# Kernel optimization log

Measured on AMD Instinct MI355X. Metric: run time of the kernel, lower is better.

## Reference

```python
import jax, jax.numpy as jnp
import numpy as np

D_STATE = 16
D_CONV = 4
TOKEN = 8
GROUPS = 4
EPS = 1e-5


def _gn(x, w, b):
    # GroupNorm(GROUPS) over [B,C,H,W]
    B, C, H, W = x.shape
    xr = x.reshape(B, GROUPS, C // GROUPS, H * W)
    mu = xr.mean((2, 3), keepdims=True)
    var = xr.var((2, 3), keepdims=True)
    xn = ((xr - mu) * jax.lax.rsqrt(var + EPS)).reshape(B, C, H, W)
    return xn * w[None, :, None, None] + b[None, :, None, None]


def _mamba(x, in_w, conv_w, conv_b, xp_w, dt_w, dt_b, A_log, Dp, out_w, dt_rank):
    # mamba_ssm Mamba forward: x [B, L, d_model]
    Bn, L, _ = x.shape
    d_inner = conv_w.shape[0]
    xz = jnp.einsum('bld,ed->ble', x, in_w)          # [B,L,2*d_inner]
    xc, z = jnp.split(xz, 2, axis=-1)
    # causal depthwise conv1d (pad left d_conv-1)
    xt = jnp.pad(jnp.transpose(xc, (0, 2, 1)), ((0, 0), (0, 0), (D_CONV - 1, 0)))
    xt = jax.lax.conv_general_dilated(xt, conv_w[:, None, :], (1,), 'VALID',
                                      dimension_numbers=('NCH', 'OIH', 'NCH'),
                                      feature_group_count=d_inner)
    xc = jax.nn.silu(jnp.transpose(xt, (0, 2, 1)) + conv_b)
    dbl = jnp.einsum('ble,fe->blf', xc, xp_w)        # [B,L,dt_rank+2*d_state]
    dt = dbl[..., :dt_rank]
    Bm = dbl[..., dt_rank:dt_rank + D_STATE]
    Cm = dbl[..., dt_rank + D_STATE:]
    delta = jax.nn.softplus(jnp.einsum('blr,er->ble', dt, dt_w) + dt_b)
    A = -jnp.exp(A_log)                              # [d_inner, d_state]

    def step(h, inp):
        u_t, d_t, b_t, c_t = inp                     # [B,d_inner],[B,d_inner],[B,d_state],[B,d_state]
        dA = jnp.exp(d_t[..., None] * A)
        h = h * dA + (d_t * u_t)[..., None] * b_t[:, None, :]
        return h, jnp.sum(h * c_t[:, None, :], axis=-1)

    xs = (jnp.transpose(xc, (1, 0, 2)), jnp.transpose(delta, (1, 0, 2)),
          jnp.transpose(Bm, (1, 0, 2)), jnp.transpose(Cm, (1, 0, 2)))
    h0 = jnp.zeros((Bn, d_inner, D_STATE), x.dtype)
    _, ys = jax.lax.scan(step, h0, xs)
    y = (jnp.transpose(ys, (1, 0, 2)) + xc * Dp) * jax.nn.silu(z)
    return jnp.einsum('ble,de->bld', y, out_w)


def _mamba_params(key, d_model, dt_rank):
    d_inner = 2 * d_model
    ks = jax.random.split(key, 5)
    p = {}
    p['in_w'] = jax.random.normal(ks[0], (2 * d_inner, d_model)) / np.sqrt(d_model).astype(np.float32)
    p['conv_w'] = jax.random.normal(ks[1], (d_inner, D_CONV)) * 0.3
    p['conv_b'] = jnp.zeros((d_inner,))
    p['xp_w'] = jax.random.normal(ks[2], (dt_rank + 2 * D_STATE, d_inner)) / np.sqrt(d_inner).astype(np.float32)
    p['dt_w'] = jax.random.normal(ks[3], (d_inner, dt_rank)) / np.sqrt(dt_rank).astype(np.float32)
    p['dt_b'] = jnp.full((d_inner,), float(np.log(np.expm1(0.01))))
    p['A_log'] = jnp.log(jnp.broadcast_to(jnp.arange(1, D_STATE + 1, dtype=jnp.float32), (d_inner, D_STATE)))
    p['D'] = jnp.ones((d_inner,))
    p['out_w'] = jax.random.normal(ks[4], (d_model, d_inner)) / np.sqrt(d_inner).astype(np.float32)
    return p


def setup_inputs() -> dict:
    key = jax.random.key(0)
    k1, k2, k3 = jax.random.split(key, 3)
    B, C, H, W = 2, 64, 128, 128
    inp = {'x': jax.random.normal(k1, (B, C, H, W), dtype=jnp.float32)}
    spa = _mamba_params(k2, C, 4)
    spe = _mamba_params(k3, C // TOKEN, 1)
    for n, p in (('spa', spa), ('spe', spe)):
        for k, v in p.items():
            inp[f'{n}_{k}'] = v
    inp['spa_gn_w'] = jnp.ones((C,)); inp['spa_gn_b'] = jnp.zeros((C,))
    inp['spe_gn_w'] = jnp.ones((C,)); inp['spe_gn_b'] = jnp.zeros((C,))
    inp['fuse_w'] = jnp.full((2,), 0.5)
    return inp


def reference(x, spa_in_w, spa_conv_w, spa_conv_b, spa_xp_w, spa_dt_w, spa_dt_b,
              spa_A_log, spa_D, spa_out_w, spe_in_w, spe_conv_w, spe_conv_b,
              spe_xp_w, spe_dt_w, spe_dt_b, spe_A_log, spe_D, spe_out_w,
              spa_gn_w, spa_gn_b, spe_gn_w, spe_gn_b, fuse_w):
    B, C, H, W = x.shape
    # SpaMamba: scan over flattened spatial sequence
    xs = jnp.transpose(x, (0, 2, 3, 1)).reshape(B, H * W, C)
    ys = _mamba(xs, spa_in_w, spa_conv_w, spa_conv_b, spa_xp_w, spa_dt_w, spa_dt_b,
                spa_A_log, spa_D, spa_out_w, 4)
    spa = jnp.transpose(ys.reshape(B, H, W, C), (0, 3, 1, 2))
    spa = jax.nn.silu(_gn(spa, spa_gn_w, spa_gn_b)) + x
    # SpeMamba: scan over channel tokens per pixel (C == TOKEN * gc, no padding)
    gc = C // TOKEN
    xe = jnp.transpose(x, (0, 2, 3, 1)).reshape(B * H * W, TOKEN, gc)
    ye = _mamba(xe, spe_in_w, spe_conv_w, spe_conv_b, spe_xp_w, spe_dt_w, spe_dt_b,
                spe_A_log, spe_D, spe_out_w, 1)
    spe = jnp.transpose(ye.reshape(B, H, W, C), (0, 3, 1, 2))
    spe = jax.nn.silu(_gn(spe, spe_gn_w, spe_gn_b)) + x
    w = jax.nn.softmax(fuse_w)
    return spa * w[0] + spe * w[1] + x
```

## Files before the change

kernel.cpp:

```cpp
#include <hip/hip_runtime.h>
#include <math.h>


#define NB 2
#define NC 64
#define HW_ 16384
#define SCH 512
#define SLC 32

__device__ __forceinline__ float sigmoidf_(float v) { return 1.f / (1.f + __expf(-v)); }
__device__ __forceinline__ float siluf_(float v)    { return v * sigmoidf_(v); }
__device__ __forceinline__ float softplusf_(float v) {
    return v > 0.f ? v + log1pf(__expf(-v)) : log1pf(__expf(v));
}

#define K1_XS_OFF 4480
#define K1_XS_STR 68
#define K1_XCL_STR 132

__global__ __launch_bounds__(256) void k1_spatial_pre(
    const float* __restrict__ x, const float* __restrict__ in_w,
    const float* __restrict__ conv_w, const float* __restrict__ conv_b,
    const float* __restrict__ xp_w, const float* __restrict__ dt_w,
    const float* __restrict__ dt_b, const float* __restrict__ A_log,
    float* __restrict__ xc_g, float* __restrict__ sz_g,
    float* __restrict__ dtp_g, float* __restrict__ Bm_g, float* __restrict__ Cm_g,
    float* __restrict__ cumA_g, float* __restrict__ hsum_g)
{
    __shared__ __align__(16) float smem[6860];
    __shared__ __align__(16) float sB[32 * 16];
    __shared__ __align__(16) float sdt[32 * 4];
    const int tid = threadIdx.x;
    const int b   = blockIdx.x >> 9;
    const int l0  = (blockIdx.x & 511) << 5;

    for (int i = tid; i < 35 * 64; i += 256) {
        int c = i / 35;
        int tok = i - c * 35;
        int l = l0 + tok - 3;
        float v = (l >= 0) ? x[((size_t)b * NC + c) * HW_ + l] : 0.f;
        smem[K1_XS_OFF + tok * K1_XS_STR + c] = v;
    }
    __syncthreads();

    {
        const int e = tid & 127;
        const int half = tid >> 7;
        float w[64];
        #pragma unroll
        for (int q = 0; q < 16; ++q) {
            float4 wv = *(const float4*)(in_w + e * 64 + q * 4);
            w[q*4] = wv.x; w[q*4+1] = wv.y; w[q*4+2] = wv.z; w[q*4+3] = wv.w;
        }
        int t0 = half ? 18 : 0, t1 = half ? 35 : 18;
        for (int tok = t0; tok < t1; ++tok) {
            const float4* xr = (const float4*)(smem + K1_XS_OFF + tok * K1_XS_STR);
            float acc = 0.f;
            #pragma unroll
            for (int q = 0; q < 16; ++q) {
                float4 xv = xr[q];
                acc += w[q*4]*xv.x + w[q*4+1]*xv.y + w[q*4+2]*xv.z + w[q*4+3]*xv.w;
            }
            smem[tok * 128 + e] = acc;
        }
        #pragma unroll
        for (int q = 0; q < 16; ++q) {
            float4 wv = *(const float4*)(in_w + (128 + e) * 64 + q * 4);
            w[q*4] = wv.x; w[q*4+1] = wv.y; w[q*4+2] = wv.z; w[q*4+3] = wv.w;
        }
        int z0 = half * 16;
        for (int tok = z0; tok < z0 + 16; ++tok) {
            const float4* xr = (const float4*)(smem + K1_XS_OFF + (tok + 3) * K1_XS_STR);
            float acc = 0.f;
            #pragma unroll
            for (int q = 0; q < 16; ++q) {
                float4 xv = xr[q];
                acc += w[q*4]*xv.x + w[q*4+1]*xv.y + w[q*4+2]*xv.z + w[q*4+3]*xv.w;
            }
            sz_g[((size_t)(b * HW_ + l0 + tok)) * 128 + e] = siluf_(acc);
        }
    }
    __syncthreads();

    {
        const int e = tid & 127;
        float cw0 = conv_w[e*4], cw1 = conv_w[e*4+1], cw2 = conv_w[e*4+2], cw3 = conv_w[e*4+3];
        float cb = conv_b[e];
        float r[16];
        #pragma unroll
        for (int k = 0; k < 16; ++k) {
            int tok = (tid + k * 256) >> 7;
            float v = cb + cw0 * smem[(tok+0)*128 + e] + cw1 * smem[(tok+1)*128 + e]
                         + cw2 * smem[(tok+2)*128 + e] + cw3 * smem[(tok+3)*128 + e];
            v = siluf_(v);
            r[k] = v;
            xc_g[((size_t)(b * HW_ + l0 + tok)) * 128 + e] = v;
        }
        __syncthreads();
        #pragma unroll
        for (int k = 0; k < 16; ++k) {
            int tok = (tid + k * 256) >> 7;
            smem[tok * K1_XCL_STR + e] = r[k];
        }
    }
    __syncthreads();

    for (int i = tid; i < 32 * 32; i += 256) {
        int tok = i >> 5;
        int f = i & 31;
        const float4* xr = (const float4*)(smem + tok * K1_XCL_STR);
        const float4* wr = (const float4*)(xp_w + (4 + f) * 128);
        float acc = 0.f;
        #pragma unroll
        for (int q = 0; q < 32; ++q) {
            float4 a = xr[q], w4 = wr[q];
            acc += a.x*w4.x + a.y*w4.y + a.z*w4.z + a.w*w4.w;
        }
        size_t row = (size_t)(b * HW_ + l0 + tok);
        if (f < 16) { Bm_g[row * 16 + f] = acc; sB[tok * 16 + f] = acc; }
        else        Cm_g[row * 16 + (f - 16)] = acc;
    }
    if (tid < 128) {
        int tok = tid >> 2;
        const float4* xr = (const float4*)(smem + tok * K1_XCL_STR);
        const float4* wr = (const float4*)(xp_w + (tid & 3) * 128);
        float acc = 0.f;
        #pragma unroll
        for (int q = 0; q < 32; ++q) {
            float4 a = xr[q], w4 = wr[q];
            acc += a.x*w4.x + a.y*w4.y + a.z*w4.z + a.w*w4.w;
        }
        dtp_g[(size_t)(b * HW_ + l0) * 4 + tid] = acc;
        sdt[tid] = acc;
    }
    __syncthreads();

    {
        const int e = tid >> 1;
        const int n0 = (tid & 1) * 8;
        float A[8];
        #pragma unroll
        for (int j = 0; j < 8; ++j) A[j] = -__expf(A_log[e * 16 + n0 + j]);
        float4 wdt = *(const float4*)(dt_w + e * 4);
        float dtb = dt_b[e];
        float h[8], cA[8];
        #pragma unroll
        for (int j = 0; j < 8; ++j) { h[j] = 0.f; cA[j] = 1.f; }
        for (int t = 0; t < 32; ++t) {
            float4 dv = *(const float4*)(sdt + t * 4);
            float d = softplusf_(wdt.x*dv.x + wdt.y*dv.y + wdt.z*dv.z + wdt.w*dv.w + dtb);
            float u = smem[t * K1_XCL_STR + e];
            float4 b0 = *(const float4*)(sB + t * 16 + n0);
            float4 b1 = *(const float4*)(sB + t * 16 + n0 + 4);
            float Bv[8]; *(float4*)(Bv) = b0; *(float4*)(Bv + 4) = b1;
            float du = d * u;
            #pragma unroll
            for (int j = 0; j < 8; ++j) {
                float dA = __expf(d * A[j]);
                h[j] = h[j] * dA + du * Bv[j];
                cA[j] *= dA;
            }
        }
        size_t so = (size_t)blockIdx.x * 2048 + tid * 8;
        *(float4*)(cumA_g + so)     = *(float4*)(cA);
        *(float4*)(cumA_g + so + 4) = *(float4*)(cA + 4);
        *(float4*)(hsum_g + so)     = *(float4*)(h);
        *(float4*)(hsum_g + so + 4) = *(float4*)(h + 4);
    }
}

__global__ __launch_bounds__(256) void k3_combine(
    const float* __restrict__ cumA_g, const float* __restrict__ hsum_g,
    float* __restrict__ Hin_g)
{
    int gid = blockIdx.x * 256 + threadIdx.x;
    int b = gid >> 11;
    int en = gid & 2047;
    float st = 0.f;
    size_t o = (size_t)b * SCH * 2048 + en;
    for (int cb = 0; cb < SCH; cb += 16) {
        float a[16], hs[16];
        #pragma unroll
        for (int k = 0; k < 16; ++k) {
            a[k]  = cumA_g[o + (size_t)k * 2048];
            hs[k] = hsum_g[o + (size_t)k * 2048];
        }
        #pragma unroll
        for (int k = 0; k < 16; ++k) {
            Hin_g[o + (size_t)k * 2048] = st;
            st = st * a[k] + hs[k];
        }
        o += (size_t)16 * 2048;
    }
}

__global__ __launch_bounds__(256) void k4_scan2(
    const float* __restrict__ xc_g, const float* __restrict__ sz_g,
    const float* __restrict__ Bm_g, const float* __restrict__ Cm_g,
    const float* __restrict__ dtp_g, const float* __restrict__ dt_w,
    const float* __restrict__ dt_b, const float* __restrict__ A_log,
    const float* __restrict__ Dp, const float* __restrict__ Hin_g,
    const float* __restrict__ out_w,
    float* __restrict__ spa_raw, float* __restrict__ part_spa)
{
    __shared__ __align__(16) float lds[9344];
    float* su  = lds;
    float* sB  = lds + 4096;
    float* sC  = lds + 4608;
    float* sdt = lds + 5120;
    float* yt  = lds + 5248;
    float* ot  = lds;
    __shared__ float wred[32];
    const int tid = threadIdx.x;
    const int b = blockIdx.x >> 9;
    const int ch = blockIdx.x & 511;
    const size_t rowbase = (size_t)b * HW_ + ch * SLC;

    const float4* u4 = (const float4*)(xc_g + rowbase * 128);
    #pragma unroll
    for (int j = 0; j < 4; ++j) ((float4*)su)[tid + j * 256] = u4[tid + j * 256];
    if (tid < 128) ((float4*)sB)[tid] = ((const float4*)(Bm_g + rowbase * 16))[tid];
    else           ((float4*)sC)[tid - 128] = ((const float4*)(Cm_g + rowbase * 16))[tid - 128];
    if (tid < 32)  ((float4*)sdt)[tid] = ((const float4*)(dtp_g + rowbase * 4))[tid];

    const int e = tid >> 1;
    const int nh = tid & 1;
    const int n0 = nh * 8;
    float A[8];
    #pragma unroll
    for (int j = 0; j < 8; ++j) A[j] = -__expf(A_log[e * 16 + n0 + j]);
    float4 wdt = *(const float4*)(dt_w + e * 4);
    float dtb = dt_b[e];
    float Dv = Dp[e];
    float h[8];
    size_t so = (size_t)blockIdx.x * 2048 + tid * 8;
    *(float4*)(h)     = *(const float4*)(Hin_g + so);
    *(float4*)(h + 4) = *(const float4*)(Hin_g + so + 4);
    __syncthreads();

    for (int t = 0; t < SLC; ++t) {
        float4 dv = *(const float4*)(sdt + t * 4);
        float d = softplusf_(wdt.x*dv.x + wdt.y*dv.y + wdt.z*dv.z + wdt.w*dv.w + dtb);
        float u = su[t * 128 + e];
        float4 b0 = *(const float4*)(sB + t * 16 + n0);
        float4 b1 = *(const float4*)(sB + t * 16 + n0 + 4);
        float4 c0 = *(const float4*)(sC + t * 16 + n0);
        float4 c1 = *(const float4*)(sC + t * 16 + n0 + 4);
        float Bv[8]; *(float4*)(Bv) = b0; *(float4*)(Bv + 4) = b1;
        float Cv[8]; *(float4*)(Cv) = c0; *(float4*)(Cv + 4) = c1;
        float du = d * u;
        float y = 0.f;
        #pragma unroll
        for (int j = 0; j < 8; ++j) {
            float dA = __expf(d * A[j]);
            h[j] = h[j] * dA + du * Bv[j];
            y += h[j] * Cv[j];
        }
        y += __shfl_xor(y, 1, 64);
        if (nh == 0) yt[t * 128 + e] = y + u * Dv;
    }
    __syncthreads();

    {
        const float4* sz4 = (const float4*)(sz_g + rowbase * 128);
        #pragma unroll
        for (int j = 0; j < 4; ++j) {
            int f = tid + j * 256;
            float4 yv = ((float4*)yt)[f];
            float4 sv = sz4[f];
            yv.x *= sv.x; yv.y *= sv.y; yv.z *= sv.z; yv.w *= sv.w;
            ((float4*)yt)[f] = yv;
        }
    }
    __syncthreads();

    for (int i = tid; i < 64 * SLC; i += 256) {
        int c = i & 63, t = i >> 6;
        const float4* wr = (const float4*)(out_w + c * 128);
        const float4* yr = (const float4*)(yt + t * 128);
        float acc = 0.f;
        #pragma unroll
        for (int q = 0; q < 32; ++q) {
            float4 w4 = wr[q], yv4 = yr[q];
            acc += w4.x*yv4.x + w4.y*yv4.y + w4.z*yv4.z + w4.w*yv4.w;
        }
        ot[c * 33 + t] = acc;
    }
    __syncthreads();

    for (int i = tid; i < 64 * SLC; i += 256) {
        int c = i >> 5, t = i & 31;
        spa_raw[((size_t)b * NC + c) * HW_ + ch * SLC + t] = ot[c * 33 + t];
    }
    float s[4], s2[4];
    #pragma unroll
    for (int g = 0; g < 4; ++g) {
        float a = 0.f, a2 = 0.f;
        for (int i = tid; i < 512; i += 256) {
            int c = 16 * g + (i >> 5), t = i & 31;
            float v = ot[c * 33 + t];
            a += v; a2 += v * v;
        }
        s[g] = a; s2[g] = a2;
    }
    #pragma unroll
    for (int g = 0; g < 4; ++g) {
        #pragma unroll
        for (int o = 1; o < 64; o <<= 1) {
            s[g]  += __shfl_xor(s[g], o, 64);
            s2[g] += __shfl_xor(s2[g], o, 64);
        }
    }
    if ((tid & 63) == 0) {
        int w = tid >> 6;
        #pragma unroll
        for (int g = 0; g < 4; ++g) { wred[w*8 + g*2] = s[g]; wred[w*8 + g*2 + 1] = s2[g]; }
    }
    __syncthreads();
    if (tid < 8)
        part_spa[tid * 1024 + blockIdx.x] = wred[tid] + wred[8+tid] + wred[16+tid] + wred[24+tid];
}

#define K5_STR 144

__global__ __launch_bounds__(256, 2) void k5_spectral(
    const float* __restrict__ x, const float* __restrict__ in_w,
    const float* __restrict__ conv_w, const float* __restrict__ conv_b,
    const float* __restrict__ xp_w, const float* __restrict__ dt_w,
    const float* __restrict__ dt_b, const float* __restrict__ A_log,
    const float* __restrict__ Dp, const float* __restrict__ out_w,
    float* __restrict__ spe_raw, float* __restrict__ part_spe)
{
    __shared__ __align__(16) float lds[7936];
    float* xcs  = lds;
    float* sBn  = lds + 2304;
    float* sCn  = lds + 4608;
    float* souw = lds + 6912;
    float* xin  = sBn;
    float* ys   = xcs;
    float* outs = sCn;
    __shared__ float wred[32];
    const int tid = threadIdx.x;
    const int b = blockIdx.x >> 10;
    const int hw0 = (blockIdx.x & 1023) << 4;
    const int s = tid >> 4;
    const int l = tid & 15;

    for (int i = tid; i < 1024; i += 256) {
        int c = i >> 4, j = i & 15;
        xin[j * 68 + c] = x[((size_t)b * NC + c) * HW_ + hw0 + j];
        souw[i] = out_w[i];
    }
    float wi0[8], wi1[8];
    #pragma unroll
    for (int c = 0; c < 8; ++c) { wi0[c] = in_w[l*8 + c]; wi1[c] = in_w[(l+16)*8 + c]; }
    float cw0 = conv_w[l*4], cw1 = conv_w[l*4+1], cw2 = conv_w[l*4+2], cw3 = conv_w[l*4+3];
    float cb = conv_b[l];
    float dtw = dt_w[l], dtb = dt_b[l];
    float wdt[16], wB[16], wC[16];
    #pragma unroll
    for (int e = 0; e < 16; ++e) {
        wdt[e] = xp_w[e];
        wB[e]  = xp_w[(1 + l) * 16 + e];
        wC[e]  = xp_w[(17 + l) * 16 + e];
    }
    __syncthreads();

    float pre[8], sz[8];
    #pragma unroll
    for (int t = 0; t < 8; ++t) {
        float4 x0 = *(const float4*)(xin + s * 68 + t * 8);
        float4 x1 = *(const float4*)(xin + s * 68 + t * 8 + 4);
        float a0 = wi0[0]*x0.x + wi0[1]*x0.y + wi0[2]*x0.z + wi0[3]*x0.w
                 + wi0[4]*x1.x + wi0[5]*x1.y + wi0[6]*x1.z + wi0[7]*x1.w;
        float a1 = wi1[0]*x0.x + wi1[1]*x0.y + wi1[2]*x0.z + wi1[3]*x0.w
                 + wi1[4]*x1.x + wi1[5]*x1.y + wi1[6]*x1.z + wi1[7]*x1.w;
        pre[t] = a0; sz[t] = siluf_(a1);
    }
    float xcv[8];
    #pragma unroll
    for (int t = 0; t < 8; ++t) {
        float v = cb + cw3 * pre[t];
        if (t >= 1) v += cw2 * pre[t-1];
        if (t >= 2) v += cw1 * pre[t-2];
        if (t >= 3) v += cw0 * pre[t-3];
        xcv[t] = siluf_(v);
    }
    #pragma unroll
    for (int t = 0; t < 8; ++t) xcs[s * K5_STR + t * 16 + l] = xcv[t];
    __syncthreads();

    float del[8];
    #pragma unroll
    for (int t = 0; t < 8; ++t) {
        const float4* xr = (const float4*)(xcs + s * K5_STR + t * 16);
        float4 v0 = xr[0], v1 = xr[1], v2 = xr[2], v3 = xr[3];
        float bn = wB[0]*v0.x + wB[1]*v0.y + wB[2]*v0.z + wB[3]*v0.w
                 + wB[4]*v1.x + wB[5]*v1.y + wB[6]*v1.z + wB[7]*v1.w
                 + wB[8]*v2.x + wB[9]*v2.y + wB[10]*v2.z + wB[11]*v2.w
                 + wB[12]*v3.x + wB[13]*v3.y + wB[14]*v3.z + wB[15]*v3.w;
        float cn = wC[0]*v0.x + wC[1]*v0.y + wC[2]*v0.z + wC[3]*v0.w
                 + wC[4]*v1.x + wC[5]*v1.y + wC[6]*v1.z + wC[7]*v1.w
                 + wC[8]*v2.x + wC[9]*v2.y + wC[10]*v2.z + wC[11]*v2.w
                 + wC[12]*v3.x + wC[13]*v3.y + wC[14]*v3.z + wC[15]*v3.w;
        float d0 = wdt[0]*v0.x + wdt[1]*v0.y + wdt[2]*v0.z + wdt[3]*v0.w
                 + wdt[4]*v1.x + wdt[5]*v1.y + wdt[6]*v1.z + wdt[7]*v1.w
                 + wdt[8]*v2.x + wdt[9]*v2.y + wdt[10]*v2.z + wdt[11]*v2.w
                 + wdt[12]*v3.x + wdt[13]*v3.y + wdt[14]*v3.z + wdt[15]*v3.w;
        sBn[s * K5_STR + t * 16 + l] = bn;
        sCn[s * K5_STR + t * 16 + l] = cn;
        del[t] = softplusf_(d0 * dtw + dtb);
    }
    __syncthreads();

    float A[16];
    #pragma unroll
    for (int n = 0; n < 16; ++n) A[n] = -__expf(A_log[l * 16 + n]);
    float Dv = Dp[l];
    float h[16];
    #pragma unroll
    for (int n = 0; n < 16; ++n) h[n] = 0.f;
    #pragma unroll
    for (int t = 0; t < 8; ++t) {
        float d = del[t], u = xcv[t];
        float du = d * u;
        float y = 0.f;
        const float4* Bp = (const float4*)(sBn + s * K5_STR + t * 16);
        const float4* Cp = (const float4*)(sCn + s * K5_STR + t * 16);
        #pragma unroll
        for (int q = 0; q < 4; ++q) {
            float4 Bq = Bp[q], Cq = Cp[q];
            float dA;
            dA = __expf(d*A[4*q+0]); h[4*q+0] = h[4*q+0]*dA + du*Bq.x; y += h[4*q+0]*Cq.x;
            dA = __expf(d*A[4*q+1]); h[4*q+1] = h[4*q+1]*dA + du*Bq.y; y += h[4*q+1]*Cq.y;
            dA = __expf(d*A[4*q+2]); h[4*q+2] = h[4*q+2]*dA + du*Bq.z; y += h[4*q+2]*Cq.z;
            dA = __expf(d*A[4*q+3]); h[4*q+3] = h[4*q+3]*dA + du*Bq.w; y += h[4*q+3]*Cq.w;
        }
        ys[s * K5_STR + t * 16 + l] = (y + u * Dv) * sz[t];
    }
    __syncthreads();

    {
        int t = l >> 1;
        int db = (l & 1) * 4;
        const float4* yr = (const float4*)(ys + s * K5_STR + t * 16);
        float4 y0 = yr[0], y1 = yr[1], y2 = yr[2], y3 = yr[3];
        #pragma unroll
        for (int jj = 0; jj < 4; ++jj) {
            int dd = db + jj;
            const float4* wr = (const float4*)(souw + dd * 16);
            float4 w0 = wr[0], w1 = wr[1], w2 = wr[2], w3 = wr[3];
            float acc = w0.x*y0.x + w0.y*y0.y + w0.z*y0.z + w0.w*y0.w
                      + w1.x*y1.x + w1.y*y1.y + w1.z*y1.z + w1.w*y1.w
                      + w2.x*y2.x + w2.y*y2.y + w2.z*y2.z + w2.w*y2.w
                      + w3.x*y3.x + w3.y*y3.y + w3.z*y3.z + w3.w*y3.w;
            outs[(t * 8 + dd) * 17 + s] = acc;
        }
    }
    __syncthreads();

    float sg[4], sg2[4];
    #pragma unroll
    for (int k = 0; k < 4; ++k) {
        int i = tid + k * 256;
        int c = i >> 4, j = i & 15;
        float v = outs[c * 17 + j];
        spe_raw[((size_t)b * NC + c) * HW_ + hw0 + j] = v;
        sg[k] = v; sg2[k] = v * v;
    }
    #pragma unroll
    for (int k = 0; k < 4; ++k) {
        #pragma unroll
        for (int o = 1; o < 64; o <<= 1) {
            sg[k]  += __shfl_xor(sg[k], o, 64);
            sg2[k] += __shfl_xor(sg2[k], o, 64);
        }
    }
    if ((tid & 63) == 0) {
        int w = tid >> 6;
        #pragma unroll
        for (int k = 0; k < 4; ++k) { wred[w*8 + k*2] = sg[k]; wred[w*8 + k*2 + 1] = sg2[k]; }
    }
    __syncthreads();
    if (tid < 8)
        part_spe[tid * 2048 + blockIdx.x] = wred[tid] + wred[8+tid] + wred[16+tid] + wred[24+tid];
}

__global__ __launch_bounds__(256) void k5b_stats(
    const float* __restrict__ part_spa, const float* __restrict__ part_spe,
    float* __restrict__ stats)
{
    __shared__ float fina[16], fine_[16];
    const int tid = threadIdx.x;
    const int combo = tid >> 4;
    const int ln = tid & 15;
    const int slot = combo & 7, bb = combo >> 3;
    {
        const float4* p = (const float4*)(part_spa + slot * 1024 + bb * 512);
        float a = 0.f;
        #pragma unroll
        for (int k = 0; k < 8; ++k) {
            float4 v = p[ln * 8 + k];
            a += v.x + v.y + v.z + v.w;
        }
        #pragma unroll
        for (int o = 1; o < 16; o <<= 1) a += __shfl_xor(a, o, 64);
        if (ln == 0) fina[combo] = a;
    }
    {
        const float4* p = (const float4*)(part_spe + slot * 2048 + bb * 1024);
        float a = 0.f;
        #pragma unroll
        for (int k = 0; k < 16; ++k) {
            float4 v = p[ln * 16 + k];
            a += v.x + v.y + v.z + v.w;
        }
        #pragma unroll
        for (int o = 1; o < 16; o <<= 1) a += __shfl_xor(a, o, 64);
        if (ln == 0) fine_[combo] = a;
    }
    __syncthreads();
    if (tid < 16) {
        int branch = tid >> 3, bb2 = (tid >> 2) & 1, g = tid & 3;
        const float* fin = branch ? fine_ : fina;
        float S  = fin[bb2 * 8 + g * 2];
        float S2 = fin[bb2 * 8 + g * 2 + 1];
        const float N = 262144.f;
        float mu = S / N;
        float var = S2 / N - mu * mu;
        stats[tid * 2] = mu;
        stats[tid * 2 + 1] = rsqrtf(var + 1e-5f);
    }
}

__global__ __launch_bounds__(256) void k6_fuse(
    const float* __restrict__ x, const float* __restrict__ spa_raw,
    const float* __restrict__ spe_raw, const float* __restrict__ stats,
    const float* __restrict__ gwa, const float* __restrict__ gba,
    const float* __restrict__ gwe, const float* __restrict__ gbe,
    const float* __restrict__ fw, float* __restrict__ out)
{
    size_t i4 = (size_t)blockIdx.x * 256 + threadIdx.x;
    size_t base = i4 * 4;
    int b = (int)(base >> 20);
    int rem = (int)(base & 1048575);
    int c = rem >> 14;
    int g = c >> 4;
    int sidx = (b * 4 + g) * 2;
    float ma = stats[sidx],      ra = stats[sidx + 1];
    float me = stats[16 + sidx], re = stats[16 + sidx + 1];
    float wa = gwa[c], ba = gba[c], we = gwe[c], be = gbe[c];
    float f0 = fw[0], f1 = fw[1];
    float mx = fmaxf(f0, f1);
    float e0 = __expf(f0 - mx), e1 = __expf(f1 - mx);
    float inv = 1.f / (e0 + e1);
    float w0 = e0 * inv, w1 = e1 * inv;
    float4 xv = *(const float4*)(x + base);
    float4 av = *(const float4*)(spa_raw + base);
    float4 ev = *(const float4*)(spe_raw + base);
    float xr[4] = {xv.x, xv.y, xv.z, xv.w};
    float ar[4] = {av.x, av.y, av.z, av.w};
    float er[4] = {ev.x, ev.y, ev.z, ev.w};
    float orr[4];
    #pragma unroll
    for (int k = 0; k < 4; ++k) {
        float spa = siluf_((ar[k] - ma) * ra * wa + ba) + xr[k];
        float spe = siluf_((er[k] - me) * re * we + be) + xr[k];
        orr[k] = spa * w0 + spe * w1 + xr[k];
    }
    float4 ov = {orr[0], orr[1], orr[2], orr[3]};
    *(float4*)(out + base) = ov;
}

extern "C" void kernel_launch(void* const* d_in, const int* in_sizes, int n_in,
                              void* d_out, int out_size, void* d_ws, size_t ws_size,
                              hipStream_t stream)
{
    const float* x      = (const float*)d_in[0];
    const float* a_inw  = (const float*)d_in[1];
    const float* a_cw   = (const float*)d_in[2];
    const float* a_cb   = (const float*)d_in[3];
    const float* a_xp   = (const float*)d_in[4];
    const float* a_dtw  = (const float*)d_in[5];
    const float* a_dtb  = (const float*)d_in[6];
    const float* a_Alog = (const float*)d_in[7];
    const float* a_D    = (const float*)d_in[8];
    const float* a_ow   = (const float*)d_in[9];
    const float* e_inw  = (const float*)d_in[10];
    const float* e_cw   = (const float*)d_in[11];
    const float* e_cb   = (const float*)d_in[12];
    const float* e_xp   = (const float*)d_in[13];
    const float* e_dtw  = (const float*)d_in[14];
    const float* e_dtb  = (const float*)d_in[15];
    const float* e_Alog = (const float*)d_in[16];
    const float* e_D    = (const float*)d_in[17];
    const float* e_ow   = (const float*)d_in[18];
    const float* gwa    = (const float*)d_in[19];
    const float* gba    = (const float*)d_in[20];
    const float* gwe    = (const float*)d_in[21];
    const float* gbe    = (const float*)d_in[22];
    const float* fw     = (const float*)d_in[23];

    float* ws    = (float*)d_ws;
    float* xc    = ws;
    float* sz    = xc    + 4194304;
    float* Bm    = sz    + 4194304;
    float* Cm    = Bm    + 524288;
    float* dtp   = Cm    + 524288;
    float* cumA  = dtp   + 131072;
    float* hsum  = cumA  + 2097152;
    float* Hin   = hsum  + 2097152;
    float* spa_r = Hin   + 2097152;
    float* spe_r = spa_r + 2097152;
    float* pspa  = spe_r + 2097152;
    float* pspe  = pspa  + 8192;
    float* stats = pspe  + 16384;

    k1_spatial_pre<<<1024, 256, 0, stream>>>(x, a_inw, a_cw, a_cb, a_xp, a_dtw,
                                             a_dtb, a_Alog,
                                             xc, sz, dtp, Bm, Cm, cumA, hsum);
    k3_combine<<<16, 256, 0, stream>>>(cumA, hsum, Hin);
    k5_spectral<<<2048, 256, 0, stream>>>(x, e_inw, e_cw, e_cb, e_xp, e_dtw, e_dtb,
                                          e_Alog, e_D, e_ow, spe_r, pspe);
    k4_scan2<<<1024, 256, 0, stream>>>(xc, sz, Bm, Cm, dtp, a_dtw, a_dtb, a_Alog,
                                       a_D, Hin, a_ow, spa_r, pspa);
    k5b_stats<<<1, 256, 0, stream>>>(pspa, pspe, stats);
    k6_fuse<<<2048, 256, 0, stream>>>(x, spa_r, spe_r, stats, gwa, gba, gwe, gbe, fw,
                                      (float*)d_out);
}
```

Baseline: 361.2 us.

## Pre-transpose input to token-major layout and register-block small projections

Adds a transpose kernel that writes x as [B,HW,C] so the spatial pre-kernel and spectral kernel read contiguous float4 rows instead of strided per-channel gathers. The in_proj stage now loads both the xc and z weight sets into registers and computes both outputs from one row load. The x_proj and out_proj matmuls are register-blocked (2x2 and 2x4 outputs per thread). Hin now aliases cumA in place, which frees workspace for xT. This adds an extra kernel launch and about 8MB of extra memory traffic, and holding 128 weights per thread raises register pressure.

```diff
diff --git a/kernel.cpp b/kernel.cpp
--- a/kernel.cpp
+++ b/kernel.cpp
@@ -13,13 +13,47 @@
 __device__ __forceinline__ float softplusf_(float v) {
     return v > 0.f ? v + log1pf(__expf(-v)) : log1pf(__expf(v));
 }
-
-#define K1_XS_OFF 4480
-#define K1_XS_STR 68
+__device__ __forceinline__ float dot4_(float4 a, float4 b) {
+    return a.x*b.x + a.y*b.y + a.z*b.z + a.w*b.w;
+}
+
+__global__ __launch_bounds__(256) void k0_transpose(
+    const float* __restrict__ x, float* __restrict__ xT)
+{
+    __shared__ __align__(16) float tile[64 * 68];
+    const int tid = threadIdx.x;
+    const int b  = blockIdx.x >> 8;
+    const int l0 = (blockIdx.x & 255) << 6;
+    {
+        int c = tid >> 2, lq = tid & 3;
+        const float4* src = (const float4*)(x + ((size_t)b * NC + c) * HW_ + l0);
+        #pragma unroll
+        for (int j = 0; j < 4; ++j) {
+            float4 v = src[lq + j * 4];
+            *(float4*)(tile + c * 68 + (lq + j * 4) * 4) = v;
+        }
+    }
+    __syncthreads();
+    {
+        int l = tid >> 2, cq = tid & 3;
+        float4* dst = (float4*)(xT + ((size_t)b * HW_ + l0 + l) * 64);
+        #pragma unroll
+        for (int j = 0; j < 4; ++j) {
+            int c4 = cq + j * 4;
+            float4 v;
+            v.x = tile[(c4 * 4 + 0) * 68 + l];
+            v.y = tile[(c4 * 4 + 1) * 68 + l];
+            v.z = tile[(c4 * 4 + 2) * 68 + l];
+            v.w = tile[(c4 * 4 + 3) * 68 + l];
+            dst[c4] = v;
+        }
+    }
+}
+
 #define K1_XCL_STR 132
 
 __global__ __launch_bounds__(256) void k1_spatial_pre(
-    const float* __restrict__ x, const float* __restrict__ in_w,
+    const float* __restrict__ xT, const float* __restrict__ in_w,
     const float* __restrict__ conv_w, const float* __restrict__ conv_b,
     const float* __restrict__ xp_w, const float* __restrict__ dt_w,
     const float* __restrict__ dt_b, const float* __restrict__ A_log,
@@ -27,57 +61,46 @@
     float* __restrict__ dtp_g, float* __restrict__ Bm_g, float* __restrict__ Cm_g,
     float* __restrict__ cumA_g, float* __restrict__ hsum_g)
 {
-    __shared__ __align__(16) float smem[6860];
-    __shared__ __align__(16) float sB[32 * 16];
-    __shared__ __align__(16) float sdt[32 * 4];
+    __shared__ __align__(16) float smem[4480];
+    __shared__ __align__(16) float sB[512];
+    __shared__ __align__(16) float sdt[128];
     const int tid = threadIdx.x;
     const int b   = blockIdx.x >> 9;
     const int l0  = (blockIdx.x & 511) << 5;
 
-    for (int i = tid; i < 35 * 64; i += 256) {
-        int c = i / 35;
-        int tok = i - c * 35;
-        int l = l0 + tok - 3;
-        float v = (l >= 0) ? x[((size_t)b * NC + c) * HW_ + l] : 0.f;
-        smem[K1_XS_OFF + tok * K1_XS_STR + c] = v;
-    }
-    __syncthreads();
-
     {
         const int e = tid & 127;
-        const int half = tid >> 7;
-        float w[64];
+        const int th = __builtin_amdgcn_readfirstlane(threadIdx.x >> 7);
+        float wxc[64], wz[64];
         #pragma unroll
         for (int q = 0; q < 16; ++q) {
-            float4 wv = *(const float4*)(in_w + e * 64 + q * 4);
-            w[q*4] = wv.x; w[q*4+1] = wv.y; w[q*4+2] = wv.z; w[q*4+3] = wv.w;
-        }
-        int t0 = half ? 18 : 0, t1 = half ? 35 : 18;
+            float4 a = *(const float4*)(in_w + e * 64 + q * 4);
+            wxc[q*4] = a.x; wxc[q*4+1] = a.y; wxc[q*4+2] = a.z; wxc[q*4+3] = a.w;
+            float4 zz = *(const float4*)(in_w + (128 + e) * 64 + q * 4);
+            wz[q*4] = zz.x; wz[q*4+1] = zz.y; wz[q*4+2] = zz.z; wz[q*4+3] = zz.w;
+        }
+        const int t0 = th ? 18 : 0, t1 = th ? 35 : 18;
         for (int tok = t0; tok < t1; ++tok) {
-            const float4* xr = (const float4*)(smem + K1_XS_OFF + tok * K1_XS_STR);
-            float acc = 0.f;
+            const int l = l0 + tok - 3;
+            float xs[64];
+            if (l >= 0) {
+                const float4* xr = (const float4*)(xT + ((size_t)b * HW_ + l) * 64);
+                #pragma unroll
+                for (int q = 0; q < 16; ++q) *(float4*)(xs + q * 4) = xr[q];
+            } else {
+                #pragma unroll
+                for (int q = 0; q < 64; ++q) xs[q] = 0.f;
+            }
+            float pre = 0.f;
             #pragma unroll
-            for (int q = 0; q < 16; ++q) {
-                float4 xv = xr[q];
-                acc += w[q*4]*xv.x + w[q*4+1]*xv.y + w[q*4+2]*xv.z + w[q*4+3]*xv.w;
+            for (int k = 0; k < 64; ++k) pre += wxc[k] * xs[k];
+            smem[tok * 128 + e] = pre;
+            if (tok >= 3) {
+                float z = 0.f;
+                #pragma unroll
+                for (int k = 0; k < 64; ++k) z += wz[k] * xs[k];
+                sz_g[((size_t)(b * HW_ + l0 + tok - 3)) * 128 + e] = siluf_(z);
             }
-            smem[tok * 128 + e] = acc;
-        }
-        #pragma unroll
-        for (int q = 0; q < 16; ++q) {
-            float4 wv = *(const float4*)(in_w + (128 + e) * 64 + q * 4);
-            w[q*4] = wv.x; w[q*4+1] = wv.y; w[q*4+2] = wv.z; w[q*4+3] = wv.w;
-        }
-        int z0 = half * 16;
-        for (int tok = z0; tok < z0 + 16; ++tok) {
-            const float4* xr = (const float4*)(smem + K1_XS_OFF + (tok + 3) * K1_XS_STR);
-            float acc = 0.f;
-            #pragma unroll
-            for (int q = 0; q < 16; ++q) {
-                float4 xv = xr[q];
-                acc += w[q*4]*xv.x + w[q*4+1]*xv.y + w[q*4+2]*xv.z + w[q*4+3]*xv.w;
-            }
-            sz_g[((size_t)(b * HW_ + l0 + tok)) * 128 + e] = siluf_(acc);
         }
     }
     __syncthreads();
@@ -105,20 +128,31 @@
     }
     __syncthreads();
 
-    for (int i = tid; i < 32 * 32; i += 256) {
-        int tok = i >> 5;
-        int f = i & 31;
-        const float4* xr = (const float4*)(smem + tok * K1_XCL_STR);
-        const float4* wr = (const float4*)(xp_w + (4 + f) * 128);
-        float acc = 0.f;
+    {
+        const int f0   = (tid & 15) << 1;
+        const int tok0 = (tid >> 4) << 1;
+        const float4* x0r = (const float4*)(smem + tok0 * K1_XCL_STR);
+        const float4* x1r = (const float4*)(smem + (tok0 + 1) * K1_XCL_STR);
+        const float4* w0r = (const float4*)(xp_w + (4 + f0) * 128);
+        const float4* w1r = (const float4*)(xp_w + (5 + f0) * 128);
+        float a00 = 0.f, a01 = 0.f, a10 = 0.f, a11 = 0.f;
         #pragma unroll
         for (int q = 0; q < 32; ++q) {
-            float4 a = xr[q], w4 = wr[q];
-            acc += a.x*w4.x + a.y*w4.y + a.z*w4.z + a.w*w4.w;
-        }
-        size_t row = (size_t)(b * HW_ + l0 + tok);
-        if (f < 16) { Bm_g[row * 16 + f] = acc; sB[tok * 16 + f] = acc; }
-        else        Cm_g[row * 16 + (f - 16)] = acc;
+            float4 w0 = w0r[q], w1 = w1r[q], p0 = x0r[q], p1 = x1r[q];
+            a00 += dot4_(w0, p0); a01 += dot4_(w0, p1);
+            a10 += dot4_(w1, p0); a11 += dot4_(w1, p1);
+        }
+        size_t row0 = (size_t)(b * HW_ + l0 + tok0);
+        if (f0 < 16) {
+            Bm_g[row0 * 16 + f0]           = a00; Bm_g[row0 * 16 + f0 + 1]       = a10;
+            Bm_g[(row0 + 1) * 16 + f0]     = a01; Bm_g[(row0 + 1) * 16 + f0 + 1] = a11;
+            sB[tok0 * 16 + f0]       = a00; sB[tok0 * 16 + f0 + 1]       = a10;
+            sB[(tok0 + 1) * 16 + f0] = a01; sB[(tok0 + 1) * 16 + f0 + 1] = a11;
+        } else {
+            int g = f0 - 16;
+            Cm_g[row0 * 16 + g]           = a00; Cm_g[row0 * 16 + g + 1]       = a10;
+            Cm_g[(row0 + 1) * 16 + g]     = a01; Cm_g[(row0 + 1) * 16 + g + 1] = a11;
+        }
     }
     if (tid < 128) {
         int tok = tid >> 2;
@@ -128,7 +162,7 @@
         #pragma unroll
         for (int q = 0; q < 32; ++q) {
             float4 a = xr[q], w4 = wr[q];
-            acc += a.x*w4.x + a.y*w4.y + a.z*w4.z + a.w*w4.w;
+            acc += dot4_(a, w4);
         }
         dtp_g[(size_t)(b * HW_ + l0) * 4 + tid] = acc;
         sdt[tid] = acc;
@@ -170,8 +204,7 @@
 }
 
 __global__ __launch_bounds__(256) void k3_combine(
-    const float* __restrict__ cumA_g, const float* __restrict__ hsum_g,
-    float* __restrict__ Hin_g)
+    const float* cumA_g, const float* hsum_g, float* Hin_g)
 {
     int gid = blockIdx.x * 256 + threadIdx.x;
     int b = gid >> 11;
@@ -274,17 +307,28 @@
     }
     __syncthreads();
 
-    for (int i = tid; i < 64 * SLC; i += 256) {
-        int c = i & 63, t = i >> 6;
-        const float4* wr = (const float4*)(out_w + c * 128);
-        const float4* yr = (const float4*)(yt + t * 128);
-        float acc = 0.f;
+    {
+        const int c0 = (tid & 31) << 1;
+        const int t0 = (tid >> 5) << 2;
+        const float4* w0r = (const float4*)(out_w + c0 * 128);
+        const float4* w1r = (const float4*)(out_w + (c0 + 1) * 128);
+        float a0[4] = {0.f, 0.f, 0.f, 0.f}, a1[4] = {0.f, 0.f, 0.f, 0.f};
         #pragma unroll
         for (int q = 0; q < 32; ++q) {
-            float4 w4 = wr[q], yv4 = yr[q];
-            acc += w4.x*yv4.x + w4.y*yv4.y + w4.z*yv4.z + w4.w*yv4.w;
-        }
-        ot[c * 33 + t] = acc;
+            float4 w0 = w0r[q], w1 = w1r[q];
+            #pragma unroll
+            for (int j = 0; j < 4; ++j) {
+                float4 yv = *(const float4*)(yt + (t0 + j) * 128 + q * 4);
+                a0[j] += dot4_(w0, yv);
+                a1[j] += dot4_(w1, yv);
+            }
+        }
+        __syncthreads();
+        #pragma unroll
+        for (int j = 0; j < 4; ++j) {
+            ot[c0 * 33 + t0 + j]       = a0[j];
+            ot[(c0 + 1) * 33 + t0 + j] = a1[j];
+        }
     }
     __syncthreads();
 
@@ -324,7 +368,7 @@
 #define K5_STR 144
 
 __global__ __launch_bounds__(256, 2) void k5_spectral(
-    const float* __restrict__ x, const float* __restrict__ in_w,
+    const float* __restrict__ xT, const float* __restrict__ in_w,
     const float* __restrict__ conv_w, const float* __restrict__ conv_b,
     const float* __restrict__ xp_w, const float* __restrict__ dt_w,
     const float* __restrict__ dt_b, const float* __restrict__ A_log,
@@ -346,10 +390,11 @@
     const int s = tid >> 4;
     const int l = tid & 15;
 
-    for (int i = tid; i < 1024; i += 256) {
-        int c = i >> 4, j = i & 15;
-        xin[j * 68 + c] = x[((size_t)b * NC + c) * HW_ + hw0 + j];
-        souw[i] = out_w[i];
+    {
+        const float4* xt4 = (const float4*)(xT + ((size_t)b * HW_ + hw0) * 64);
+        int j = tid >> 4, c4 = (tid & 15) << 2;
+        *(float4*)(xin + j * 68 + c4) = xt4[tid];
+        ((float4*)souw)[tid] = ((const float4*)out_w)[tid];
     }
     float wi0[8], wi1[8];
     #pragma unroll
@@ -450,10 +495,7 @@
             int dd = db + jj;
             const float4* wr = (const float4*)(souw + dd * 16);
             float4 w0 = wr[0], w1 = wr[1], w2 = wr[2], w3 = wr[3];
-            float acc = w0.x*y0.x + w0.y*y0.y + w0.z*y0.z + w0.w*y0.w
-                      + w1.x*y1.x + w1.y*y1.y + w1.z*y1.z + w1.w*y1.w
-                      + w2.x*y2.x + w2.y*y2.y + w2.z*y2.z + w2.w*y2.w
-                      + w3.x*y3.x + w3.y*y3.y + w3.z*y3.z + w3.w*y3.w;
+            float acc = dot4_(w0, y0) + dot4_(w1, y1) + dot4_(w2, y2) + dot4_(w3, y3);
             outs[(t * 8 + dd) * 17 + s] = acc;
         }
     }
@@ -609,21 +651,22 @@
     float* dtp   = Cm    + 524288;
     float* cumA  = dtp   + 131072;
     float* hsum  = cumA  + 2097152;
-    float* Hin   = hsum  + 2097152;
-    float* spa_r = Hin   + 2097152;
+    float* xT    = hsum  + 2097152;
+    float* spa_r = xT    + 2097152;
     float* spe_r = spa_r + 2097152;
     float* pspa  = spe_r + 2097152;
     float* pspe  = pspa  + 8192;
     float* stats = pspe  + 16384;
 
-    k1_spatial_pre<<<1024, 256, 0, stream>>>(x, a_inw, a_cw, a_cb, a_xp, a_dtw,
+    k0_transpose<<<512, 256, 0, stream>>>(x, xT);
+    k1_spatial_pre<<<1024, 256, 0, stream>>>(xT, a_inw, a_cw, a_cb, a_xp, a_dtw,
                                              a_dtb, a_Alog,
                                              xc, sz, dtp, Bm, Cm, cumA, hsum);
-    k3_combine<<<16, 256, 0, stream>>>(cumA, hsum, Hin);
-    k5_spectral<<<2048, 256, 0, stream>>>(x, e_inw, e_cw, e_cb, e_xp, e_dtw, e_dtb,
+    k3_combine<<<16, 256, 0, stream>>>(cumA, hsum, cumA);
+    k5_spectral<<<2048, 256, 0, stream>>>(xT, e_inw, e_cw, e_cb, e_xp, e_dtw, e_dtb,
                                           e_Alog, e_D, e_ow, spe_r, pspe);
     k4_scan2<<<1024, 256, 0, stream>>>(xc, sz, Bm, Cm, dtp, a_dtw, a_dtb, a_Alog,
-                                       a_D, Hin, a_ow, spa_r, pspa);
+                                       a_D, cumA, a_ow, spa_r, pspa);
     k5b_stats<<<1, 256, 0, stream>>>(pspa, pspe, stats);
     k6_fuse<<<2048, 256, 0, stream>>>(x, spa_r, spe_r, stats, gwa, gba, gwe, gbe, fw,
                                       (float*)d_out);
```

Measured after the change: 360.0 us. No clear change (-0.3%).
